# Kernel optimization log

Measured on AMD Instinct MI355X. Metric: run time of the kernel, lower is better.

The kernel has to match this reference:

```python
import jax, jax.numpy as jnp
import numpy as np

BSZ = 2          # batch
H_IMG = 180      # BEV height
W_IMG = 180      # BEV width
BLK = 15         # block_size
D = 128          # d_model
NH = 8           # nhead
DH = D // NH     # head dim


def _bn_relu(x, g, b, m, v, eps=1e-5):
    # eval-mode BatchNorm2d followed by ReLU; x is NCHW
    s = g * jax.lax.rsqrt(v + eps)
    return jax.nn.relu((x - m[None, :, None, None]) * s[None, :, None, None]
                       + b[None, :, None, None])


def _split_tokens(x):
    # (B,C,H,W) -> (B*nb, blk*blk, C), block order = (row-block, col-block)
    B, C, H, W = x.shape
    hb, wb = H // BLK, W // BLK
    x = x.reshape(B, C, hb, BLK, wb, BLK)
    x = x.transpose(0, 2, 4, 1, 3, 5)              # (B,hb,wb,C,blk,blk)
    x = x.reshape(B * hb * wb, C, BLK * BLK)
    return x.transpose(0, 2, 1)                    # (B*nb, L, C)


def _merge_tokens(t, B, H, W):
    # (B*nb, L, C) -> (B,C,H,W), inverse of _split_tokens
    hb, wb = H // BLK, W // BLK
    C = t.shape[-1]
    x = t.transpose(0, 2, 1).reshape(B, hb, wb, C, BLK, BLK)
    x = x.transpose(0, 3, 1, 4, 2, 5)              # (B,C,hb,blk,wb,blk)
    return x.reshape(B, C, H, W)


def setup_inputs() -> dict:
    key = jax.random.key(0)
    ks = jax.random.split(key, 16)
    n = lambda i, shp, sc=0.05: jax.random.normal(ks[i], shp, jnp.float32) * sc
    inp = {
        'camera_feat': jax.random.normal(ks[0], (BSZ, 80, H_IMG, W_IMG), jnp.float32),
        'lidar_feat': jax.random.normal(ks[1], (BSZ, 256, H_IMG, W_IMG), jnp.float32),
        'cam_w': n(2, (D, 80)),
        'cam_gamma': jnp.ones((D,), jnp.float32),
        'cam_beta': jnp.zeros((D,), jnp.float32),
        'cam_mean': n(3, (D,)),
        'cam_var': jax.random.uniform(ks[4], (D,), jnp.float32, 0.5, 1.5),
        'lidar_w': n(5, (D, 256)),
        'lidar_gamma': jnp.ones((D,), jnp.float32),
        'lidar_beta': jnp.zeros((D,), jnp.float32),
        'lidar_mean': n(6, (D,)),
        'lidar_var': jax.random.uniform(ks[7], (D,), jnp.float32, 0.5, 1.5),
        'in_proj_w': n(8, (3 * D, D)),
        'in_proj_b': jnp.zeros((3 * D,), jnp.float32),
        'out_proj_w': n(9, (D, D)),
        'out_proj_b': jnp.zeros((D,), jnp.float32),
        'outc_w': n(10, (256, D, 3, 3)),
        'outc_gamma': jnp.ones((256,), jnp.float32),
        'outc_beta': jnp.zeros((256,), jnp.float32),
        'outc_mean': n(11, (256,)),
        'outc_var': jax.random.uniform(ks[12], (256,), jnp.float32, 0.5, 1.5),
    }
    return inp


def reference(camera_feat, lidar_feat,
              cam_w, cam_gamma, cam_beta, cam_mean, cam_var,
              lidar_w, lidar_gamma, lidar_beta, lidar_mean, lidar_var,
              in_proj_w, in_proj_b, out_proj_w, out_proj_b,
              outc_w, outc_gamma, outc_beta, outc_mean, outc_var):
    B, _, H, W = camera_feat.shape
    # 1x1 conv projections + BN + ReLU
    cam_p = _bn_relu(jnp.einsum('bchw,dc->bdhw', camera_feat, cam_w),
                     cam_gamma, cam_beta, cam_mean, cam_var)
    lid_p = _bn_relu(jnp.einsum('bchw,dc->bdhw', lidar_feat, lidar_w),
                     lidar_gamma, lidar_beta, lidar_mean, lidar_var)
    # windowed tokens: (B*nb, L=225, D)
    cam_t = _split_tokens(cam_p)
    lid_t = _split_tokens(lid_p)
    # cross-attention: query=lidar, key/value=camera (torch MHA math)
    wq, wk, wv = in_proj_w[:D], in_proj_w[D:2 * D], in_proj_w[2 * D:]
    bq, bk, bv = in_proj_b[:D], in_proj_b[D:2 * D], in_proj_b[2 * D:]
    BN, L, _ = lid_t.shape
    q = (lid_t @ wq.T + bq).reshape(BN, L, NH, DH).transpose(0, 2, 1, 3)
    k = (cam_t @ wk.T + bk).reshape(BN, L, NH, DH).transpose(0, 2, 1, 3)
    v = (cam_t @ wv.T + bv).reshape(BN, L, NH, DH).transpose(0, 2, 1, 3)
    scores = jnp.einsum('bhqd,bhkd->bhqk', q, k) / jnp.sqrt(jnp.float32(DH))
    attn = jax.nn.softmax(scores, axis=-1)
    ctx = jnp.einsum('bhqk,bhkd->bhqd', attn, v)
    ctx = ctx.transpose(0, 2, 1, 3).reshape(BN, L, D)
    attn_out = ctx @ out_proj_w.T + out_proj_b
    # merge windows back and fuse
    fused = _merge_tokens(attn_out, B, H, W) + lid_p
    # 3x3 conv + BN + ReLU
    y = jax.lax.conv_general_dilated(
        fused, outc_w, window_strides=(1, 1), padding='SAME',
        dimension_numbers=('NCHW', 'OIHW', 'NCHW'))
    return _bn_relu(y, outc_gamma, outc_beta, outc_mean, outc_var)
```

## Files before the change

kernel.cpp:

```cpp
#include <hip/hip_runtime.h>
#include <hip/hip_bf16.h>
#include <cmath>

#define HW      32400
#define WIMG    180
#define DD      128
#define NHEADS  8
#define DHEAD   16
#define LTOK    225
#define PSTRIDE 64928
#define FBROW   188
#define FBH     182
#define FBSZ    ((size_t)FBH * FBROW * 128)
#define QSCALE  0.36067376022224085f

typedef __attribute__((ext_vector_type(8))) short bf16x8;
typedef __attribute__((ext_vector_type(4))) float f32x4;

union U16B { uint4 u; int4 i; bf16x8 v; };

__device__ __forceinline__ bf16x8 ldfrag(const __hip_bfloat16* p, int ld, int lane) {
  return *(const bf16x8*)(p + (size_t)(lane & 15) * ld + ((lane >> 4) << 3));
}

__device__ __forceinline__ float bf2f(unsigned int u) {
  return __uint_as_float(u << 16);
}

__device__ __forceinline__ unsigned short f2bf(float x) {
  unsigned int b = __float_as_uint(x);
  return (unsigned short)((b + 0x7fffu + ((b >> 16) & 1u)) >> 16);
}

__global__ void k_cast(const float* __restrict__ in, __hip_bfloat16* __restrict__ out, int n) {
  int i = blockIdx.x * 256 + threadIdx.x;
  if (i < n) out[i] = __float2bfloat16(in[i]);
}

__global__ void k_prepproj(const float* __restrict__ w, __hip_bfloat16* __restrict__ wb,
                           int C, int Kpad) {
  int i = blockIdx.x * 256 + threadIdx.x;
  if (i >= 128 * Kpad) return;
  int d = i / Kpad, c = i % Kpad;
  wb[i] = (c < C) ? __float2bfloat16(w[d * C + c]) : __float2bfloat16(0.f);
}

__global__ void k_prepw2(const float* __restrict__ cw, __hip_bfloat16* __restrict__ wcb) {
  int i = blockIdx.x * 256 + threadIdx.x;
  if (i >= 294912) return;
  int oc16  = i / 18432;
  int r0    = i % 18432;
  int tap   = r0 / 2048;
  int r1    = r0 % 2048;
  int chunk = r1 / 512;
  int r2    = r1 % 512;
  int lane  = r2 / 8;
  int e     = r2 % 8;
  int oc = oc16 * 16 + (lane & 15);
  int ic = chunk * 32 + (lane >> 4) * 8 + e;
  wcb[i] = __float2bfloat16(cw[(size_t)(oc * 128 + ic) * 9 + tap]);
}

__global__ void k_zero_border(__hip_bfloat16* __restrict__ fbb) {
  int idx = blockIdx.x * 256 + threadIdx.x;
  if (idx >= 2 * 736 * 16) return;
  int b = idx / (736 * 16);
  int r = idx % (736 * 16);
  int px = r >> 4, blk = r & 15;
  int row, col;
  if (px < 188)      { row = 0;            col = px; }
  else if (px < 376) { row = 181;          col = px - 188; }
  else if (px < 556) { row = px - 376 + 1; col = 0; }
  else               { row = px - 556 + 1; col = 181; }
  ((uint4*)(fbb + (size_t)b * FBSZ + ((size_t)row * FBROW + col) * 128))[blk] =
      make_uint4(0u, 0u, 0u, 0u);
}

__global__ void __launch_bounds__(256) k_proj_mfma(
    const float* __restrict__ in, const __hip_bfloat16* __restrict__ wb,
    const float* __restrict__ g, const float* __restrict__ be,
    const float* __restrict__ mu, const float* __restrict__ var,
    __hip_bfloat16* __restrict__ outp, int C, int Kpad) {
  __shared__ __align__(16) __hip_bfloat16 sa[128 * 64];
  int m0 = blockIdx.x * 128;
  int b = blockIdx.z;
  int tid = threadIdx.x, lane = tid & 63, wid = tid >> 6;
  int wm = (wid >> 1) * 64, wn = (wid & 1) * 64;
  const float* inb = in + (size_t)b * C * HW;
  int sp = (tid >> 1) & 127;
  int sc4 = (tid & 1) * 4;
  int gp = m0 + sp;
  bool pok = gp < HW;
  f32x4 acc[4][4] = {};
  for (int kc = 0; kc < Kpad; kc += 64) {
    __syncthreads();
#pragma unroll
    for (int it = 0; it < 8; ++it) {
      int lc = sc4 + it * 8;
      int c = kc + lc;
      unsigned short u[4];
#pragma unroll
      for (int j = 0; j < 4; ++j) {
        float x = (pok && (c + j) < C) ? inb[(size_t)(c + j) * HW + gp] : 0.f;
        u[j] = f2bf(x);
      }
      int blk = (lc >> 3) ^ (sp & 7);
      char* dst = (char*)sa + sp * 128 + blk * 16 + (lc & 7) * 2;
      *(uint2*)dst = make_uint2(((unsigned)u[1] << 16) | u[0],
                                ((unsigned)u[3] << 16) | u[2]);
    }
    __syncthreads();
#pragma unroll
    for (int ks = 0; ks < 2; ++ks) {
      bf16x8 af[4], bfr[4];
#pragma unroll
      for (int i = 0; i < 4; ++i) {
        int pr = wm + i * 16 + (lane & 15);
        int blk = ((ks * 4 + (lane >> 4)) ^ (pr & 7));
        af[i] = *(const bf16x8*)((const char*)sa + pr * 128 + blk * 16);
      }
#pragma unroll
      for (int j = 0; j < 4; ++j)
        bfr[j] = ldfrag(wb + (size_t)(wn + j * 16) * Kpad + kc + ks * 32, Kpad, lane);
#pragma unroll
      for (int i = 0; i < 4; ++i)
#pragma unroll
        for (int j = 0; j < 4; ++j)
          acc[i][j] = __builtin_amdgcn_mfma_f32_16x16x32_bf16(af[i], bfr[j], acc[i][j], 0, 0, 0);
    }
  }
  int col = lane & 15, rq = lane >> 4;
  __hip_bfloat16* ob = outp + (size_t)b * PSTRIDE * 128;
#pragma unroll
  for (int j = 0; j < 4; ++j) {
    int d = wn + j * 16 + col;
    float s = g[d] * rsqrtf(var[d] + 1e-5f);
    float mm = mu[d], bb = be[d];
#pragma unroll
    for (int i = 0; i < 4; ++i) {
#pragma unroll
      for (int r = 0; r < 4; ++r) {
        int m = m0 + wm + i * 16 + rq * 4 + r;
        if (m < HW) {
          float y = (acc[i][j][r] - mm) * s + bb;
          ob[(size_t)m * 128 + d] = __float2bfloat16(fmaxf(y, 0.f));
        }
      }
    }
  }
}

__global__ void __launch_bounds__(256) k_gemm_bias(
    const __hip_bfloat16* __restrict__ A, const __hip_bfloat16* __restrict__ B,
    const float* __restrict__ bias, __hip_bfloat16* __restrict__ out,
    int K, int ldout, float oscale) {
  int m0 = blockIdx.x * 128, n0 = blockIdx.y * 128, b = blockIdx.z;
  int lane = threadIdx.x & 63, wid = threadIdx.x >> 6;
  int wm = (wid >> 1) * 64, wn = (wid & 1) * 64;
  const __hip_bfloat16* Ab = A + (size_t)b * PSTRIDE * K;
  f32x4 acc[4][4] = {};
  for (int kc = 0; kc < K; kc += 32) {
    bf16x8 af[4], bfr[4];
#pragma unroll
    for (int i = 0; i < 4; ++i)
      af[i] = ldfrag(Ab + (size_t)(m0 + wm + i * 16) * K + kc, K, lane);
#pragma unroll
    for (int j = 0; j < 4; ++j)
      bfr[j] = ldfrag(B + (size_t)(n0 + wn + j * 16) * K + kc, K, lane);
#pragma unroll
    for (int i = 0; i < 4; ++i)
#pragma unroll
      for (int j = 0; j < 4; ++j)
        acc[i][j] = __builtin_amdgcn_mfma_f32_16x16x32_bf16(af[i], bfr[j], acc[i][j], 0, 0, 0);
  }
  int col = lane & 15, rq = lane >> 4;
  __hip_bfloat16* ob = out + (size_t)b * PSTRIDE * ldout;
#pragma unroll
  for (int j = 0; j < 4; ++j) {
    int n = n0 + wn + j * 16 + col;
    float bs = bias[n];
#pragma unroll
    for (int i = 0; i < 4; ++i) {
#pragma unroll
      for (int r = 0; r < 4; ++r) {
        int m = m0 + wm + i * 16 + rq * 4 + r;
        if (m < HW) ob[(size_t)m * ldout + n] = __float2bfloat16((acc[i][j][r] + bs) * oscale);
      }
    }
  }
}

__global__ void __launch_bounds__(256) k_attn_mfma(
    const __hip_bfloat16* __restrict__ qc, const __hip_bfloat16* __restrict__ kvb,
    __hip_bfloat16* __restrict__ ctx) {
  __shared__ __align__(16) uint4 Kf[15 * 64];
  __shared__ __align__(16) uint4 Vf[15 * 64];
  __shared__ __align__(16) unsigned short psh[4 * 384];
  int bn = blockIdx.x, hh = blockIdx.y;
  int b = bn / 144, rr = bn % 144, tby = rr / 12, tbx = rr % 12;
  int tid = threadIdx.x;
  int pbase = tby * 15 * WIMG + tbx * 15;
  const __hip_bfloat16* kvbase = kvb + (size_t)b * PSTRIDE * 256 + hh * 16;

  if (tid < 240) {
    int row = tid;
    int ck = row >> 4, q = row & 15;
    uint4 k0 = make_uint4(0, 0, 0, 0), k1 = k0, v0 = k0, v1 = k0;
    if (row < LTOK) {
      int p = pbase + (row / 15) * WIMG + (row % 15);
      const uint4* kp = (const uint4*)(kvbase + (size_t)p * 256);
      k0 = kp[0]; k1 = kp[1];
      v0 = kp[16]; v1 = kp[17];
    }
    uint4 zz = make_uint4(0, 0, 0, 0);
    Kf[ck * 64 + q]      = k0;
    Kf[ck * 64 + 16 + q] = k1;
    Kf[ck * 64 + 32 + q] = zz;
    Kf[ck * 64 + 48 + q] = zz;
    unsigned short vv[16];
    *(uint4*)&vv[0] = v0;
    *(uint4*)&vv[8] = v1;
    int vg = q >> 3, vj = q & 7;
#pragma unroll
    for (int d0 = 0; d0 < 16; ++d0) {
      int d = (d0 + q + 2 * ck) & 15;
      ((unsigned short*)&Vf[ck * 64 + vg * 16 + d])[vj] = vv[d];
    }
    Vf[ck * 64 + 32 + q] = zz;
    Vf[ck * 64 + 48 + q] = zz;
  }
  __syncthreads();

  int lane = tid & 63, wid = tid >> 6;
  int g = lane >> 4, q15 = lane & 15;
  int wq0 = wid * 64;
  char* pw_base = (char*)psh + wid * 768;
  const bf16x8* KfB = (const bf16x8*)Kf + lane;
  const bf16x8* VfB = (const bf16x8*)Vf + lane;

  bf16x8 qf[4];
#pragma unroll
  for (int i = 0; i < 4; ++i) {
    int q = wq0 + i * 16 + q15;
    int qq = q < LTOK ? q : 0;
    int p = pbase + (qq / 15) * WIMG + (qq % 15);
    U16B u; u.u = make_uint4(0, 0, 0, 0);
    if (g < 2) u.u = *(const uint4*)(qc + ((size_t)b * PSTRIDE + p) * 128 + hh * 16 + g * 8);
    qf[i] = u.v;
  }

  const f32x4 zacc = {};
  float ls[4] = {0.f, 0.f, 0.f, 0.f};
  f32x4 oac[4] = {};
#pragma unroll 1
  for (int ck = 0; ck < 15; ++ck) {
    bf16x8 kf = KfB[ck * 64];
    bf16x8 vf = VfB[ck * 64];
#pragma unroll
    for (int i = 0; i < 4; ++i) {
      f32x4 st = __builtin_amdgcn_mfma_f32_16x16x32_bf16(kf, qf[i], zacc, 0, 0, 0);
      float p0 = exp2f(st[0]);
      float p1 = exp2f(st[1]);
      float p2 = exp2f(st[2]);
      float p3 = exp2f(st[3]);
      if (ck == 14) {
        if (g) p0 = 0.f;
        p1 = 0.f; p2 = 0.f; p3 = 0.f;
      }
      ls[i] += (p0 + p1) + (p2 + p3);
      unsigned w0 = (unsigned)__bfloat16_as_ushort(__float2bfloat16(p0)) |
                    ((unsigned)__bfloat16_as_ushort(__float2bfloat16(p1)) << 16);
      unsigned w1 = (unsigned)__bfloat16_as_ushort(__float2bfloat16(p2)) |
                    ((unsigned)__bfloat16_as_ushort(__float2bfloat16(p3)) << 16);
      *(uint2*)(pw_base + q15 * 48 + g * 8) = make_uint2(w0, w1);
      U16B pu;
      pu.u = *(const uint4*)(pw_base + q15 * 48 + (g & 1) * 16);
      oac[i] = __builtin_amdgcn_mfma_f32_16x16x32_bf16(vf, pu.v, oac[i], 0, 0, 0);
    }
  }
#pragma unroll
  for (int i = 0; i < 4; ++i) {
    ls[i] += __shfl_xor(ls[i], 16);
    ls[i] += __shfl_xor(ls[i], 32);
  }

  __hip_bfloat16* cb = ctx + (size_t)b * PSTRIDE * 128 + hh * 16;
#pragma unroll
  for (int i = 0; i < 4; ++i) {
    float inv = 1.f / ls[i];
    int qo = wq0 + i * 16 + q15;
    if (qo < LTOK) {
      unsigned lo = (unsigned)f2bf(oac[i][0] * inv) | ((unsigned)f2bf(oac[i][1] * inv) << 16);
      unsigned hi = (unsigned)f2bf(oac[i][2] * inv) | ((unsigned)f2bf(oac[i][3] * inv) << 16);
      int p = pbase + (qo / 15) * WIMG + (qo % 15);
      *(uint2*)(cb + (size_t)p * 128 + g * 4) = make_uint2(lo, hi);
    }
  }
}

__global__ void __launch_bounds__(256) k_outproj_mfma(
    const __hip_bfloat16* __restrict__ ctx, const __hip_bfloat16* __restrict__ wob,
    const float* __restrict__ opb, const __hip_bfloat16* __restrict__ lidb,
    __hip_bfloat16* __restrict__ fb) {
  int m0 = blockIdx.x * 128, b = blockIdx.z;
  int lane = threadIdx.x & 63, wid = threadIdx.x >> 6;
  int wm = (wid >> 1) * 64, wn = (wid & 1) * 64;
  const __hip_bfloat16* Ab = ctx + (size_t)b * PSTRIDE * 128;
  f32x4 acc[4][4] = {};
  for (int kc = 0; kc < 128; kc += 32) {
    bf16x8 af[4], bfr[4];
#pragma unroll
    for (int i = 0; i < 4; ++i)
      af[i] = ldfrag(Ab + (size_t)(m0 + wm + i * 16) * 128 + kc, 128, lane);
#pragma unroll
    for (int j = 0; j < 4; ++j)
      bfr[j] = ldfrag(wob + (size_t)(wn + j * 16) * 128 + kc, 128, lane);
#pragma unroll
    for (int i = 0; i < 4; ++i)
#pragma unroll
      for (int j = 0; j < 4; ++j)
        acc[i][j] = __builtin_amdgcn_mfma_f32_16x16x32_bf16(af[i], bfr[j], acc[i][j], 0, 0, 0);
  }
  int col = lane & 15, rq = lane >> 4;
  const __hip_bfloat16* lb = lidb + (size_t)b * PSTRIDE * 128;
  __hip_bfloat16* fbp = fb + (size_t)b * FBSZ;
#pragma unroll
  for (int j = 0; j < 4; ++j) {
    int n = wn + j * 16 + col;
    float bs = opb[n];
#pragma unroll
    for (int i = 0; i < 4; ++i) {
#pragma unroll
      for (int r = 0; r < 4; ++r) {
        int m = m0 + wm + i * 16 + rq * 4 + r;
        if (m < HW) {
          float v = acc[i][j][r] + bs + __bfloat162float(lb[(size_t)m * 128 + n]);
          int hhh = m / WIMG, www = m % WIMG;
          fbp[((size_t)(hhh + 1) * FBROW + (www + 1)) * 128 + n] = __float2bfloat16(v);
        }
      }
    }
  }
}

__global__ void __launch_bounds__(512) k_conv_mfma(
    const __hip_bfloat16* __restrict__ fb, const __hip_bfloat16* __restrict__ wcb,
    const float* __restrict__ g, const float* __restrict__ be,
    const float* __restrict__ mu, const float* __restrict__ var,
    float* __restrict__ out) {
  __shared__ __align__(16) uint4 Asm[2976];
  int bx = blockIdx.x;
  int h = bx / 3, strip = bx % 3;
  int w0 = strip * 60;
  int b = blockIdx.z;
  int tid = threadIdx.x, lane = tid & 63, wid = tid >> 6;
  int q15 = lane & 15, kg = lane >> 4;
  int wpx = (wid & 1) * 32;
  int ocq = wid >> 1;
  const __hip_bfloat16* fbb = fb + (size_t)b * FBSZ;
  const __hip_bfloat16* Bw = wcb + (size_t)(ocq * 4) * 18432 + lane * 8;

#pragma unroll
  for (int it = 0; it < 6; ++it) {
    int slot = it * 512 + tid;
    if (slot < 2976) {
      int px = slot % 62;
      int rowk = slot / 62;
      int dy = rowk >> 4, kgrp = rowk & 15;
      Asm[slot] = *(const uint4*)(fbb + ((size_t)(h + dy) * FBROW + (w0 + px)) * 128 + kgrp * 8);
    }
  }

#define LOADB(dst, t)                                                          \
  {                                                                            \
    int tap_ = (t) >> 2, ch_ = (t) & 3;                                        \
    _Pragma("unroll") for (int j = 0; j < 4; ++j)                              \
        dst[j] = *(const bf16x8*)(Bw + (size_t)j * 18432 + tap_ * 2048 + ch_ * 512); \
  }

  bf16x8 bp0[4], bp1[4], bp2[4];
  LOADB(bp0, 0);
  LOADB(bp1, 1);
  LOADB(bp2, 2);
  __syncthreads();

  f32x4 acc[2][4] = {};

#define STEP(t, bp)                                                            \
  {                                                                            \
    int tap_ = (t) >> 2, ch_ = (t) & 3;                                        \
    int dy_ = tap_ / 3, dx_ = tap_ % 3;                                        \
    int rowk_ = (dy_ * 16 + ch_ * 4 + kg) * 62;                                \
    bf16x8 af[2];                                                              \
    _Pragma("unroll") for (int i = 0; i < 2; ++i)                              \
        af[i] = *(const bf16x8*)&Asm[rowk_ + wpx + i * 16 + q15 + dx_];        \
    _Pragma("unroll") for (int i = 0; i < 2; ++i)                              \
        _Pragma("unroll") for (int j = 0; j < 4; ++j)                          \
            acc[i][j] = __builtin_amdgcn_mfma_f32_16x16x32_bf16(af[i], bp[j], acc[i][j], 0, 0, 0); \
  }

#pragma unroll
  for (int t = 0; t < 36; t += 3) {
    STEP(t, bp0);
    if (t + 3 < 36) LOADB(bp0, t + 3);
    STEP(t + 1, bp1);
    if (t + 4 < 36) LOADB(bp1, t + 4);
    STEP(t + 2, bp2);
    if (t + 5 < 36) LOADB(bp2, t + 5);
  }
#undef STEP
#undef LOADB

  int ocbase = ocq * 64;
#pragma unroll
  for (int j = 0; j < 4; ++j) {
    int oc = ocbase + j * 16 + q15;
    float s = g[oc] * rsqrtf(var[oc] + 1e-5f);
    float mm = mu[oc], bb = be[oc];
#pragma unroll
    for (int i = 0; i < 2; ++i) {
      int pxb = wpx + i * 16 + kg * 4;
      if (pxb < 60) {
        float4 o4;
        o4.x = fmaxf((acc[i][j][0] - mm) * s + bb, 0.f);
        o4.y = fmaxf((acc[i][j][1] - mm) * s + bb, 0.f);
        o4.z = fmaxf((acc[i][j][2] - mm) * s + bb, 0.f);
        o4.w = fmaxf((acc[i][j][3] - mm) * s + bb, 0.f);
        *(float4*)(&out[(size_t)(b * 256 + oc) * HW + h * WIMG + w0 + pxb]) = o4;
      }
    }
  }
}

extern "C" void kernel_launch(void* const* d_in, const int* in_sizes, int n_in,
                              void* d_out, int out_size, void* d_ws, size_t ws_size,
                              hipStream_t stream) {
  const float* camera = (const float*)d_in[0];
  const float* lidar  = (const float*)d_in[1];
  const float* cam_w  = (const float*)d_in[2];
  const float* cam_g  = (const float*)d_in[3];
  const float* cam_b  = (const float*)d_in[4];
  const float* cam_m  = (const float*)d_in[5];
  const float* cam_v  = (const float*)d_in[6];
  const float* lid_w  = (const float*)d_in[7];
  const float* lid_g  = (const float*)d_in[8];
  const float* lid_b  = (const float*)d_in[9];
  const float* lid_m  = (const float*)d_in[10];
  const float* lid_v  = (const float*)d_in[11];
  const float* ipw    = (const float*)d_in[12];
  const float* ipb    = (const float*)d_in[13];
  const float* opw    = (const float*)d_in[14];
  const float* opb    = (const float*)d_in[15];
  const float* ocw    = (const float*)d_in[16];
  const float* ocg    = (const float*)d_in[17];
  const float* ocb    = (const float*)d_in[18];
  const float* ocm    = (const float*)d_in[19];
  const float* ocv    = (const float*)d_in[20];

  __hip_bfloat16* ws = (__hip_bfloat16*)d_ws;
  const size_t NP = (size_t)2 * PSTRIDE * 128;
  __hip_bfloat16* cam_bf = ws;
  __hip_bfloat16* lid_bf = ws + NP;
  __hip_bfloat16* qc     = ws + 2 * NP;
  __hip_bfloat16* kvb    = ws + 3 * NP;
  __hip_bfloat16* wipb   = ws + 5 * NP;
  __hip_bfloat16* wob    = wipb + 384 * 128;
  __hip_bfloat16* wcb    = wob + 128 * 128;
  __hip_bfloat16* wcamb  = wcb + 256 * 9 * 128;
  __hip_bfloat16* wlidb  = wcamb + 128 * 128;
  __hip_bfloat16* fbbuf  = cam_bf;

  dim3 blk(256);
  hipLaunchKernelGGL(k_cast, dim3(192), blk, 0, stream, ipw, wipb, 384 * 128);
  hipLaunchKernelGGL(k_cast, dim3(64), blk, 0, stream, opw, wob, 128 * 128);
  hipLaunchKernelGGL(k_prepw2, dim3(1152), blk, 0, stream, ocw, wcb);
  hipLaunchKernelGGL(k_prepproj, dim3(64), blk, 0, stream, cam_w, wcamb, 80, 128);
  hipLaunchKernelGGL(k_prepproj, dim3(128), blk, 0, stream, lid_w, wlidb, 256, 256);
  dim3 gproj(254, 1, 2);
  hipLaunchKernelGGL(k_proj_mfma, gproj, blk, 0, stream,
                     camera, wcamb, cam_g, cam_b, cam_m, cam_v, cam_bf, 80, 128);
  hipLaunchKernelGGL(k_proj_mfma, gproj, blk, 0, stream,
                     lidar, wlidb, lid_g, lid_b, lid_m, lid_v, lid_bf, 256, 256);
  hipLaunchKernelGGL(k_gemm_bias, dim3(254, 1, 2), blk, 0, stream,
                     lid_bf, wipb, ipb, qc, 128, 128, QSCALE);
  hipLaunchKernelGGL(k_gemm_bias, dim3(254, 2, 2), blk, 0, stream,
                     cam_bf, wipb + 128 * 128, ipb + 128, kvb, 128, 256, 1.0f);
  hipLaunchKernelGGL(k_attn_mfma, dim3(288, 8), blk, 0, stream, qc, kvb, qc);
  hipLaunchKernelGGL(k_zero_border, dim3(92), blk, 0, stream, fbbuf);
  hipLaunchKernelGGL(k_outproj_mfma, dim3(254, 1, 2), blk, 0, stream,
                     qc, wob, opb, lid_bf, fbbuf);
  hipLaunchKernelGGL(k_conv_mfma, dim3(540, 1, 2), dim3(512), 0, stream,
                     fbbuf, wcb, ocg, ocb, ocm, ocv, (float*)d_out);
}
```

Baseline: 297.0 us.

## Compute two output rows per conv block to reuse weight fragments

The 3x3 conv kernel now has each block compute two adjacent output rows, staging four padded input rows in shared memory instead of three. Each loaded weight fragment then feeds twice as many MFMAs, which roughly halves global weight traffic per output, and the grid is halved to match. In exchange, accumulator registers double and weight prefetch depth drops from three stages to two. The added launch_bounds occupancy hint could cause register spills.

```diff
diff --git a/kernel.cpp b/kernel.cpp
--- a/kernel.cpp
+++ b/kernel.cpp
@@ -343,14 +343,15 @@
   }
 }
 
-__global__ void __launch_bounds__(512) k_conv_mfma(
+__global__ void __launch_bounds__(512, 4) k_conv_mfma(
     const __hip_bfloat16* __restrict__ fb, const __hip_bfloat16* __restrict__ wcb,
     const float* __restrict__ g, const float* __restrict__ be,
     const float* __restrict__ mu, const float* __restrict__ var,
     float* __restrict__ out) {
-  __shared__ __align__(16) uint4 Asm[2976];
+  __shared__ __align__(16) uint4 Asm[4 * 16 * 62];
   int bx = blockIdx.x;
-  int h = bx / 3, strip = bx % 3;
+  int hp = bx / 3, strip = bx % 3;
+  int h0 = hp * 2;
   int w0 = strip * 60;
   int b = blockIdx.z;
   int tid = threadIdx.x, lane = tid & 63, wid = tid >> 6;
@@ -361,13 +362,13 @@
   const __hip_bfloat16* Bw = wcb + (size_t)(ocq * 4) * 18432 + lane * 8;
 
 #pragma unroll
-  for (int it = 0; it < 6; ++it) {
+  for (int it = 0; it < 8; ++it) {
     int slot = it * 512 + tid;
-    if (slot < 2976) {
+    if (slot < 3968) {
       int px = slot % 62;
       int rowk = slot / 62;
       int dy = rowk >> 4, kgrp = rowk & 15;
-      Asm[slot] = *(const uint4*)(fbb + ((size_t)(h + dy) * FBROW + (w0 + px)) * 128 + kgrp * 8);
+      Asm[slot] = *(const uint4*)(fbb + ((size_t)(h0 + dy) * FBROW + (w0 + px)) * 128 + kgrp * 8);
     }
   }
 
@@ -378,35 +379,35 @@
         dst[j] = *(const bf16x8*)(Bw + (size_t)j * 18432 + tap_ * 2048 + ch_ * 512); \
   }
 
-  bf16x8 bp0[4], bp1[4], bp2[4];
+  bf16x8 bp0[4], bp1[4];
   LOADB(bp0, 0);
   LOADB(bp1, 1);
-  LOADB(bp2, 2);
   __syncthreads();
 
-  f32x4 acc[2][4] = {};
+  f32x4 acc[2][2][4] = {};
 
 #define STEP(t, bp)                                                            \
   {                                                                            \
     int tap_ = (t) >> 2, ch_ = (t) & 3;                                        \
     int dy_ = tap_ / 3, dx_ = tap_ % 3;                                        \
-    int rowk_ = (dy_ * 16 + ch_ * 4 + kg) * 62;                                \
-    bf16x8 af[2];                                                              \
-    _Pragma("unroll") for (int i = 0; i < 2; ++i)                              \
-        af[i] = *(const bf16x8*)&Asm[rowk_ + wpx + i * 16 + q15 + dx_];        \
-    _Pragma("unroll") for (int i = 0; i < 2; ++i)                              \
-        _Pragma("unroll") for (int j = 0; j < 4; ++j)                          \
-            acc[i][j] = __builtin_amdgcn_mfma_f32_16x16x32_bf16(af[i], bp[j], acc[i][j], 0, 0, 0); \
-  }
-
-#pragma unroll
-  for (int t = 0; t < 36; t += 3) {
+    bf16x8 af[2][2];                                                           \
+    _Pragma("unroll") for (int r = 0; r < 2; ++r) {                            \
+      int rowk_ = ((dy_ + r) * 16 + ch_ * 4 + kg) * 62;                        \
+      _Pragma("unroll") for (int i = 0; i < 2; ++i)                            \
+          af[r][i] = *(const bf16x8*)&Asm[rowk_ + wpx + i * 16 + q15 + dx_];   \
+    }                                                                          \
+    _Pragma("unroll") for (int r = 0; r < 2; ++r)                              \
+        _Pragma("unroll") for (int i = 0; i < 2; ++i)                          \
+            _Pragma("unroll") for (int j = 0; j < 4; ++j)                      \
+                acc[r][i][j] = __builtin_amdgcn_mfma_f32_16x16x32_bf16(af[r][i], bp[j], acc[r][i][j], 0, 0, 0); \
+  }
+
+#pragma unroll
+  for (int t = 0; t < 36; t += 2) {
     STEP(t, bp0);
-    if (t + 3 < 36) LOADB(bp0, t + 3);
+    if (t + 2 < 36) LOADB(bp0, t + 2);
     STEP(t + 1, bp1);
-    if (t + 4 < 36) LOADB(bp1, t + 4);
-    STEP(t + 2, bp2);
-    if (t + 5 < 36) LOADB(bp2, t + 5);
+    if (t + 3 < 36) LOADB(bp1, t + 3);
   }
 #undef STEP
 #undef LOADB
@@ -418,15 +419,18 @@
     float s = g[oc] * rsqrtf(var[oc] + 1e-5f);
     float mm = mu[oc], bb = be[oc];
 #pragma unroll
-    for (int i = 0; i < 2; ++i) {
-      int pxb = wpx + i * 16 + kg * 4;
-      if (pxb < 60) {
-        float4 o4;
-        o4.x = fmaxf((acc[i][j][0] - mm) * s + bb, 0.f);
-        o4.y = fmaxf((acc[i][j][1] - mm) * s + bb, 0.f);
-        o4.z = fmaxf((acc[i][j][2] - mm) * s + bb, 0.f);
-        o4.w = fmaxf((acc[i][j][3] - mm) * s + bb, 0.f);
-        *(float4*)(&out[(size_t)(b * 256 + oc) * HW + h * WIMG + w0 + pxb]) = o4;
+    for (int r = 0; r < 2; ++r) {
+#pragma unroll
+      for (int i = 0; i < 2; ++i) {
+        int pxb = wpx + i * 16 + kg * 4;
+        if (pxb < 60) {
+          float4 o4;
+          o4.x = fmaxf((acc[r][i][j][0] - mm) * s + bb, 0.f);
+          o4.y = fmaxf((acc[r][i][j][1] - mm) * s + bb, 0.f);
+          o4.z = fmaxf((acc[r][i][j][2] - mm) * s + bb, 0.f);
+          o4.w = fmaxf((acc[r][i][j][3] - mm) * s + bb, 0.f);
+          *(float4*)(&out[(size_t)(b * 256 + oc) * HW + (h0 + r) * WIMG + w0 + pxb]) = o4;
+        }
       }
     }
   }
@@ -489,6 +493,6 @@
   hipLaunchKernelGGL(k_zero_border, dim3(92), blk, 0, stream, fbbuf);
   hipLaunchKernelGGL(k_outproj_mfma, dim3(254, 1, 2), blk, 0, stream,
                      qc, wob, opb, lid_bf, fbbuf);
-  hipLaunchKernelGGL(k_conv_mfma, dim3(540, 1, 2), dim3(512), 0, stream,
+  hipLaunchKernelGGL(k_conv_mfma, dim3(270, 1, 2), dim3(512), 0, stream,
                      fbbuf, wcb, ocg, ocb, ocm, ocv, (float*)d_out);
 }
```

Result: slower. 387.1 us (+30.3%).
